# Optimization experiments

Measured on AMD Instinct MI355X. Metric: run time of the kernel, lower is better.

Reference implementation:

```python
import jax, jax.numpy as jnp
import numpy as np

ALPHA = 0.2  # LeakyReLU negative slope (init arg alpha)


def setup_inputs() -> dict:
    key = jax.random.key(0)
    k1, k2, k3 = jax.random.split(key, 3)
    B, N, F_in, F_out = 8, 2048, 256, 256
    inp = jax.random.normal(k1, (B, N, F_in), dtype=jnp.float32)
    adj = jnp.ones((B, N, N), dtype=jnp.float32)  # unused by the module's forward
    # xavier_uniform with gain=1.414
    gain = 1.414
    bW = gain * np.sqrt(6.0 / (F_in + F_out))
    W = jax.random.uniform(k2, (F_in, F_out), minval=-bW, maxval=bW, dtype=jnp.float32)
    ba = gain * np.sqrt(6.0 / (2 * F_out + 1))
    a = jax.random.uniform(k3, (2 * F_out, 1), minval=-ba, maxval=ba, dtype=jnp.float32)
    return {"inp": inp, "adj": adj, "W": W, "a": a}


def reference(inp, adj, W, a):
    # inp: [B, N, F_in]; W: [F_in, F_out]; a: [2*F_out, 1]. adj is unused (as in source).
    F_out = W.shape[1]
    h = jnp.matmul(inp, W)  # [B, N, F_out]
    # e[b,i,j] = leakyrelu(a1 . h_i + a2 . h_j)  (equivalent to the repeat+cat+matmul)
    a1 = a[:F_out, 0]
    a2 = a[F_out:, 0]
    s1 = jnp.einsum('bnf,f->bn', h, a1)  # [B, N]
    s2 = jnp.einsum('bnf,f->bn', h, a2)  # [B, N]
    e = jax.nn.leaky_relu(s1[:, :, None] + s2[:, None, :], negative_slope=ALPHA)  # [B, N, N]
    # global per-batch min-max normalization, then affine *30 - 20
    mn = jnp.min(e, axis=(1, 2), keepdims=True)
    mx = jnp.max(e, axis=(1, 2), keepdims=True)
    e = (e - mn) / (mx - mn) * 30.0 - 20.0
    attention = jax.nn.sigmoid(e)  # dropout p=0 / eval: identity
    h_prime = jnp.matmul(attention, h)  # [B, N, F_out]
    h_prime = jax.nn.elu(h_prime)  # concat=True branch
    return h_prime, attention
```

## Files before the change

kernel.cpp:

```cpp
#include <hip/hip_runtime.h>
#include <stdint.h>

#define B_   8
#define N_   2048
#define F_   256
#define BN_  (B_ * N_)
#define ALPHA_ 0.2f

typedef __attribute__((ext_vector_type(8))) short  short8;
typedef __attribute__((ext_vector_type(4))) float  f32x4;

__device__ __forceinline__ unsigned short f2bf(float x) {
  uint32_t u = __float_as_uint(x);
  uint32_t r = (u + 0x7fffu + ((u >> 16) & 1u)) >> 16;
  return (unsigned short)r;
}

__device__ __forceinline__ uint32_t fkey(float f) {
  uint32_t b = __float_as_uint(f);
  return b ^ (uint32_t)(((int32_t)b >> 31) | (int32_t)0x80000000);
}
__device__ __forceinline__ float ikey(uint32_t k) {
  uint32_t b = (k & 0x80000000u) ? (k ^ 0x80000000u) : ~k;
  return __uint_as_float(b);
}

__device__ __forceinline__ void async_load16(const void* g, void* l) {
  __builtin_amdgcn_global_load_lds(
      (const __attribute__((address_space(1))) uint32_t*)g,
      (__attribute__((address_space(3))) uint32_t*)l, 16, 0, 0);
}

__device__ __forceinline__ void nt_store4(float* p, f32x4 v) {
  __builtin_nontemporal_store(v, (f32x4*)p);
}

__global__ void k_cvt_w(const float* __restrict__ W, unsigned short* __restrict__ WT,
                        uint32_t* __restrict__ maxk, uint32_t* __restrict__ mink) {
  int k = blockIdx.x, n = threadIdx.x;
  if (k == 0 && n < 16) { maxk[n] = 0u; mink[n] = 0xFFFFFFFFu; }
  WT[n * F_ + k] = f2bf(W[k * F_ + n]);
}

__launch_bounds__(256, 2)
__global__ void k_gemm1(const float* __restrict__ inp,
                        const unsigned short* __restrict__ WT,
                        const float* __restrict__ avec,
                        unsigned short* __restrict__ hT,
                        float* __restrict__ s1g, float* __restrict__ s2g,
                        uint32_t* __restrict__ maxk, uint32_t* __restrict__ mink) {
  __shared__ __align__(16) char smem[256 * 72 * 2];
  __shared__ float s1_lds[64], s2_lds[64];
  unsigned short* Atile = (unsigned short*)smem;
  unsigned short* Btile = (unsigned short*)(smem + 4096);

  const int tid  = threadIdx.x;
  const int wave = tid >> 6, lane = tid & 63;
  const int n16  = lane & 15, quad = lane >> 4;
  const int i0   = blockIdx.x * 64;
  const int b    = i0 >> 11;

  if (tid < 64) { s1_lds[tid] = 0.0f; s2_lds[tid] = 0.0f; }

  f32x4 acc[4][4];
  #pragma unroll
  for (int mt = 0; mt < 4; ++mt)
    #pragma unroll
    for (int nt = 0; nt < 4; ++nt) acc[mt][nt] = (f32x4){0.f, 0.f, 0.f, 0.f};

  for (int k0 = 0; k0 < F_; k0 += 32) {
    {
      int r = tid >> 2, cp = tid & 3;
      const float* gp = inp + (size_t)(i0 + r) * F_ + k0 + cp * 8;
      float4 va = *(const float4*)gp;
      float4 vb = *(const float4*)(gp + 4);
      short8 sv;
      sv[0] = (short)f2bf(va.x); sv[1] = (short)f2bf(va.y);
      sv[2] = (short)f2bf(va.z); sv[3] = (short)f2bf(va.w);
      sv[4] = (short)f2bf(vb.x); sv[5] = (short)f2bf(vb.y);
      sv[6] = (short)f2bf(vb.z); sv[7] = (short)f2bf(vb.w);
      *(short8*)((char*)Atile + r * 64 + cp * 16) = sv;
    }
    #pragma unroll
    for (int g4 = 0; g4 < 4; ++g4) {
      int f = (wave << 6) + (g4 << 4) + (lane >> 2);
      int p = lane & 3;
      async_load16(WT + (size_t)f * F_ + k0 + p * 8,
                   (char*)Btile + wave * 4096 + g4 * 1024);
    }
    __syncthreads();

    short8 af[4], bf_[4];
    #pragma unroll
    for (int mt = 0; mt < 4; ++mt)
      af[mt] = *(const short8*)((const char*)Atile + ((mt * 16 + n16) * 64 + quad * 16));
    #pragma unroll
    for (int nt = 0; nt < 4; ++nt)
      bf_[nt] = *(const short8*)((const char*)Btile + ((wave * 64 + nt * 16 + n16) * 64 + quad * 16));
    #pragma unroll
    for (int mt = 0; mt < 4; ++mt)
      #pragma unroll
      for (int nt = 0; nt < 4; ++nt)
        acc[mt][nt] = __builtin_amdgcn_mfma_f32_16x16x32_bf16(af[mt], bf_[nt], acc[mt][nt], 0, 0, 0);
    __syncthreads();
  }

  unsigned short* Trans = (unsigned short*)smem;

  #pragma unroll
  for (int mt = 0; mt < 4; ++mt)
    #pragma unroll
    for (int nt = 0; nt < 4; ++nt) {
      int f = (wave << 6) + (nt << 4) + n16;
      int i = (mt << 4) + (quad << 2);
      ushort4 pk;
      pk.x = f2bf(acc[mt][nt][0]); pk.y = f2bf(acc[mt][nt][1]);
      pk.z = f2bf(acc[mt][nt][2]); pk.w = f2bf(acc[mt][nt][3]);
      *(ushort4*)(Trans + f * 72 + i) = pk;
    }

  float a1v[4], a2v[4];
  #pragma unroll
  for (int nt = 0; nt < 4; ++nt) {
    int f = (wave << 6) + (nt << 4) + n16;
    a1v[nt] = avec[f];
    a2v[nt] = avec[F_ + f];
  }
  #pragma unroll
  for (int mt = 0; mt < 4; ++mt) {
    float s1p[4] = {0, 0, 0, 0}, s2p[4] = {0, 0, 0, 0};
    #pragma unroll
    for (int nt = 0; nt < 4; ++nt)
      #pragma unroll
      for (int rg = 0; rg < 4; ++rg) {
        s1p[rg] = fmaf(acc[mt][nt][rg], a1v[nt], s1p[rg]);
        s2p[rg] = fmaf(acc[mt][nt][rg], a2v[nt], s2p[rg]);
      }
    #pragma unroll
    for (int rg = 0; rg < 4; ++rg) {
      float v1 = s1p[rg], v2 = s2p[rg];
      #pragma unroll
      for (int off = 1; off < 16; off <<= 1) {
        v1 += __shfl_xor(v1, off);
        v2 += __shfl_xor(v2, off);
      }
      if (n16 == 0) {
        atomicAdd(&s1_lds[(mt << 4) + (quad << 2) + rg], v1);
        atomicAdd(&s2_lds[(mt << 4) + (quad << 2) + rg], v2);
      }
    }
  }
  __syncthreads();

  #pragma unroll
  for (int it = 0; it < 8; ++it) {
    int f = it * 32 + wave * 8 + (lane >> 3);
    int i = (lane & 7) * 8;
    short8 v = *(const short8*)(Trans + f * 72 + i);
    *(short8*)(hT + (size_t)f * BN_ + i0 + i) = v;
  }

  if (tid < 64) {
    float v1 = s1_lds[tid], v2 = s2_lds[tid];
    s1g[i0 + tid] = v1;
    s2g[i0 + tid] = v2;
    float mn1 = v1, mx1 = v1, mn2 = v2, mx2 = v2;
    #pragma unroll
    for (int off = 1; off < 64; off <<= 1) {
      mn1 = fminf(mn1, __shfl_xor(mn1, off));
      mx1 = fmaxf(mx1, __shfl_xor(mx1, off));
      mn2 = fminf(mn2, __shfl_xor(mn2, off));
      mx2 = fmaxf(mx2, __shfl_xor(mx2, off));
    }
    if (tid == 0) {
      atomicMax(&maxk[b * 2 + 0], fkey(mx1));
      atomicMax(&maxk[b * 2 + 1], fkey(mx2));
      atomicMin(&mink[b * 2 + 0], fkey(mn1));
      atomicMin(&mink[b * 2 + 1], fkey(mn2));
    }
  }
}

__launch_bounds__(256, 2)
__global__ void k_gemm2(const unsigned short* __restrict__ hT,
                        const float* __restrict__ s1, const float* __restrict__ s2,
                        const uint32_t* __restrict__ maxk, const uint32_t* __restrict__ mink,
                        float* __restrict__ hprime,
                        float* __restrict__ att) {
  __shared__ __align__(16) unsigned short Btile[3][256 * 32];
  __shared__ __align__(16) unsigned short Atile[2][1024];
  __shared__ __align__(16) float s2_lds[N_];

  const int tid  = threadIdx.x;
  const int wave = tid >> 6, lane = tid & 63;
  const int n16  = lane & 15, quad = lane >> 4;
  const int blk  = blockIdx.x;
  const int b    = blk & 7;
  const int i0   = (blk >> 3) * 32;

  float mx1 = ikey(maxk[b * 2 + 0]), mx2 = ikey(maxk[b * 2 + 1]);
  float mn1 = ikey(mink[b * 2 + 0]), mn2 = ikey(mink[b * 2 + 1]);
  float smn = mn1 + mn2, smx = mx1 + mx2;
  float emn = fmaxf(smn, ALPHA_ * smn);
  float emx = fmaxf(smx, ALPHA_ * smx);
  float scale  = 30.0f / (emx - emn);
  const float uscale = -scale;
  const float ubias  = emn * scale + 20.0f;

  const int r_att = tid >> 3;
  const int c_att = tid & 7;
  const float s1v = s1[b * N_ + i0 + r_att];
  const float* s2b = s2 + b * N_;
  float* attrow = att + ((size_t)(b * N_ + i0 + r_att)) * N_;

  auto stage_b = [&](int slot, int k0_) {
    #pragma unroll
    for (int g4 = 0; g4 < 4; ++g4) {
      int f = (wave << 6) + (g4 << 4) + (lane >> 2);
      int p = lane & 3;
      async_load16(hT + (size_t)f * BN_ + b * N_ + k0_ + p * 8,
                   (char*)Btile + slot * 16384 + wave * 4096 + g4 * 1024);
    }
  };

  #pragma unroll
  for (int it = 0; it < 2; ++it)
    async_load16(s2b + wave * 512 + it * 256 + lane * 4,
                 (char*)s2_lds + wave * 2048 + it * 1024);
  stage_b(0, 0);
  stage_b(1, 32);
  asm volatile("s_waitcnt vmcnt(8)" ::: "memory");
  __builtin_amdgcn_s_barrier();
  asm volatile("" ::: "memory");

  f32x4 acc[2][4];
  #pragma unroll
  for (int mt = 0; mt < 2; ++mt)
    #pragma unroll
    for (int nt = 0; nt < 4; ++nt) acc[mt][nt] = (f32x4){0.f, 0.f, 0.f, 0.f};

  int sl_r = 0, sl_n = 2;
  for (int t = 0; t < 64; ++t) {
    const int abuf = (t & 1) * 2048;
    const int k0   = t << 5;

    float4 va = *(const float4*)((const char*)s2_lds + k0 * 4 + c_att * 16);
    float v[4] = {va.x, va.y, va.z, va.w};
    #pragma unroll
    for (int jj = 0; jj < 4; ++jj) {
      float s = s1v + v[jj];
      float l = fmaxf(s, ALPHA_ * s);
      float u = fmaf(l, uscale, ubias);
      float p_ = __builtin_amdgcn_rcpf(1.0f + __expf(u));
      v[jj] = p_;
    }
    nt_store4(attrow + k0 + c_att * 4, (f32x4){v[0], v[1], v[2], v[3]});
    ushort4 spk;
    spk.x = f2bf(v[0]); spk.y = f2bf(v[1]); spk.z = f2bf(v[2]); spk.w = f2bf(v[3]);
    *(ushort4*)((char*)Atile + abuf + tid * 8) = spk;

    asm volatile("s_waitcnt vmcnt(5) lgkmcnt(0)" ::: "memory");
    __builtin_amdgcn_s_barrier();
    asm volatile("" ::: "memory");

    stage_b(sl_n, k0 + 64);

    short8 af0 = *(const short8*)((const char*)Atile + abuf + n16 * 64 + quad * 16);
    short8 af1 = *(const short8*)((const char*)Atile + abuf + (16 + n16) * 64 + quad * 16);
    short8 bf_[4];
    #pragma unroll
    for (int nt = 0; nt < 4; ++nt)
      bf_[nt] = *(const short8*)((const char*)Btile + sl_r * 16384 +
                                 (wave * 64 + nt * 16 + n16) * 64 + quad * 16);

    #pragma unroll
    for (int nt = 0; nt < 4; ++nt) {
      acc[0][nt] = __builtin_amdgcn_mfma_f32_16x16x32_bf16(af0, bf_[nt], acc[0][nt], 0, 0, 0);
      acc[1][nt] = __builtin_amdgcn_mfma_f32_16x16x32_bf16(af1, bf_[nt], acc[1][nt], 0, 0, 0);
    }

    sl_r = (sl_r == 2) ? 0 : sl_r + 1;
    sl_n = (sl_n == 2) ? 0 : sl_n + 1;
  }

  asm volatile("s_waitcnt vmcnt(0)" ::: "memory");

  float* hp = hprime + ((size_t)(b * N_ + i0)) * F_;
  #pragma unroll
  for (int mt = 0; mt < 2; ++mt)
    #pragma unroll
    for (int nt = 0; nt < 4; ++nt) {
      int fcol = (wave << 6) + (nt << 4) + n16;
      int irow = (mt << 4) + (quad << 2);
      #pragma unroll
      for (int rg = 0; rg < 4; ++rg) {
        float x = acc[mt][nt][rg];
        float y = x > 0.0f ? x : (__expf(x) - 1.0f);
        __builtin_nontemporal_store(y, hp + (size_t)(irow + rg) * F_ + fcol);
      }
    }
}

extern "C" void kernel_launch(void* const* d_in, const int* in_sizes, int n_in,
                              void* d_out, int out_size, void* d_ws, size_t ws_size,
                              hipStream_t stream) {
  const float* inp  = (const float*)d_in[0];
  const float* W    = (const float*)d_in[2];
  const float* avec = (const float*)d_in[3];

  float* hprime = (float*)d_out;
  float* att    = (float*)d_out + (size_t)B_ * N_ * F_;

  char* ws = (char*)d_ws;
  unsigned short* WT = (unsigned short*)ws;
  unsigned short* hT = (unsigned short*)(ws + 131072);
  float* s1          = (float*)(ws + 131072 + 8388608);
  float* s2          = s1 + BN_;
  uint32_t* maxk     = (uint32_t*)(s2 + BN_);
  uint32_t* mink     = maxk + 16;

  k_cvt_w<<<F_, F_, 0, stream>>>(W, WT, maxk, mink);
  k_gemm1<<<BN_ / 64, 256, 0, stream>>>(inp, WT, avec, hT, s1, s2, maxk, mink);
  k_gemm2<<<512, 256, 0, stream>>>(hT, s1, s2, maxk, mink, hprime, att);
}
```

Measured before the change: 272.7 us.

## Compute attention fragments in registers per wave, drop block barriers in gemm2 loop

Reworks the attention-times-h GEMM so each wave builds its own MFMA A-operand directly in registers from s1/s2, instead of writing bf16 attention to shared memory and synchronising the block every k-step. Each wave now owns a 16x128 output tile and stages its own private double-buffered slice of hT, which removes the per-iteration block barrier. The cost is redundant sigmoid computation, since two waves share each row and each computes the full A fragment. The sequence also becomes more serial: the next tile is loaded while only a single buffer is in flight, and waits on vmcnt(1) may expose load latency.

```diff
diff --git a/kernel.cpp b/kernel.cpp
--- a/kernel.cpp
+++ b/kernel.cpp
@@ -187,13 +187,13 @@
                         const uint32_t* __restrict__ maxk, const uint32_t* __restrict__ mink,
                         float* __restrict__ hprime,
                         float* __restrict__ att) {
-  __shared__ __align__(16) unsigned short Btile[3][256 * 32];
-  __shared__ __align__(16) unsigned short Atile[2][1024];
+  __shared__ __align__(16) char Btile[4 * 2 * 8192];
   __shared__ __align__(16) float s2_lds[N_];
 
   const int tid  = threadIdx.x;
   const int wave = tid >> 6, lane = tid & 63;
   const int n16  = lane & 15, quad = lane >> 4;
+  const int wm   = wave >> 1, wn = wave & 1;
   const int blk  = blockIdx.x;
   const int b    = blk & 7;
   const int i0   = (blk >> 3) * 32;
@@ -207,19 +207,20 @@
   const float uscale = -scale;
   const float ubias  = emn * scale + 20.0f;
 
-  const int r_att = tid >> 3;
-  const int c_att = tid & 7;
-  const float s1v = s1[b * N_ + i0 + r_att];
-  const float* s2b = s2 + b * N_;
-  float* attrow = att + ((size_t)(b * N_ + i0 + r_att)) * N_;
-
-  auto stage_b = [&](int slot, int k0_) {
-    #pragma unroll
-    for (int g4 = 0; g4 < 4; ++g4) {
-      int f = (wave << 6) + (g4 << 4) + (lane >> 2);
+  const int   myrow = 16 * wm + n16;
+  const float s1v   = s1[b * N_ + i0 + myrow];
+  const float* s2b  = s2 + b * N_;
+  float* attrow = att + ((size_t)(b * N_ + i0 + myrow)) * N_;
+
+  char* wseg = Btile + wave * 16384;
+
+  auto stage_b = [&](int buf_, int k0_) {
+    #pragma unroll
+    for (int g = 0; g < 8; ++g) {
+      int f = 128 * wn + g * 16 + (lane >> 2);
       int p = lane & 3;
       async_load16(hT + (size_t)f * BN_ + b * N_ + k0_ + p * 8,
-                   (char*)Btile + slot * 16384 + wave * 4096 + g4 * 1024);
+                   wseg + buf_ * 8192 + g * 1024);
     }
   };
 
@@ -228,77 +229,63 @@
     async_load16(s2b + wave * 512 + it * 256 + lane * 4,
                  (char*)s2_lds + wave * 2048 + it * 1024);
   stage_b(0, 0);
-  stage_b(1, 32);
   asm volatile("s_waitcnt vmcnt(8)" ::: "memory");
   __builtin_amdgcn_s_barrier();
-  asm volatile("" ::: "memory");
-
-  f32x4 acc[2][4];
-  #pragma unroll
-  for (int mt = 0; mt < 2; ++mt)
-    #pragma unroll
-    for (int nt = 0; nt < 4; ++nt) acc[mt][nt] = (f32x4){0.f, 0.f, 0.f, 0.f};
-
-  int sl_r = 0, sl_n = 2;
+  asm volatile("s_waitcnt vmcnt(0)" ::: "memory");
+
+  f32x4 acc[8];
+  #pragma unroll
+  for (int nt = 0; nt < 8; ++nt) acc[nt] = (f32x4){0.f, 0.f, 0.f, 0.f};
+
   for (int t = 0; t < 64; ++t) {
-    const int abuf = (t & 1) * 2048;
-    const int k0   = t << 5;
-
-    float4 va = *(const float4*)((const char*)s2_lds + k0 * 4 + c_att * 16);
-    float v[4] = {va.x, va.y, va.z, va.w};
-    #pragma unroll
-    for (int jj = 0; jj < 4; ++jj) {
+    const int cur = t & 1;
+    const int k0  = t << 5;
+
+    asm volatile("s_waitcnt vmcnt(1)" ::: "memory");
+
+    short8 bf_[8];
+    #pragma unroll
+    for (int nt = 0; nt < 8; ++nt)
+      bf_[nt] = *(const short8*)(wseg + cur * 8192 + (nt * 16 + n16) * 64 + quad * 16);
+
+    if (t < 63) stage_b(cur ^ 1, k0 + 32);
+
+    float4 va = *(const float4*)((const char*)s2_lds + (k0 + quad * 8) * 4);
+    float4 vb = *(const float4*)((const char*)s2_lds + (k0 + quad * 8) * 4 + 16);
+    float v[8] = {va.x, va.y, va.z, va.w, vb.x, vb.y, vb.z, vb.w};
+    #pragma unroll
+    for (int jj = 0; jj < 8; ++jj) {
       float s = s1v + v[jj];
       float l = fmaxf(s, ALPHA_ * s);
       float u = fmaf(l, uscale, ubias);
-      float p_ = __builtin_amdgcn_rcpf(1.0f + __expf(u));
-      v[jj] = p_;
-    }
-    nt_store4(attrow + k0 + c_att * 4, (f32x4){v[0], v[1], v[2], v[3]});
-    ushort4 spk;
-    spk.x = f2bf(v[0]); spk.y = f2bf(v[1]); spk.z = f2bf(v[2]); spk.w = f2bf(v[3]);
-    *(ushort4*)((char*)Atile + abuf + tid * 8) = spk;
-
-    asm volatile("s_waitcnt vmcnt(5) lgkmcnt(0)" ::: "memory");
-    __builtin_amdgcn_s_barrier();
-    asm volatile("" ::: "memory");
-
-    stage_b(sl_n, k0 + 64);
-
-    short8 af0 = *(const short8*)((const char*)Atile + abuf + n16 * 64 + quad * 16);
-    short8 af1 = *(const short8*)((const char*)Atile + abuf + (16 + n16) * 64 + quad * 16);
-    short8 bf_[4];
-    #pragma unroll
-    for (int nt = 0; nt < 4; ++nt)
-      bf_[nt] = *(const short8*)((const char*)Btile + sl_r * 16384 +
-                                 (wave * 64 + nt * 16 + n16) * 64 + quad * 16);
-
-    #pragma unroll
-    for (int nt = 0; nt < 4; ++nt) {
-      acc[0][nt] = __builtin_amdgcn_mfma_f32_16x16x32_bf16(af0, bf_[nt], acc[0][nt], 0, 0, 0);
-      acc[1][nt] = __builtin_amdgcn_mfma_f32_16x16x32_bf16(af1, bf_[nt], acc[1][nt], 0, 0, 0);
-    }
-
-    sl_r = (sl_r == 2) ? 0 : sl_r + 1;
-    sl_n = (sl_n == 2) ? 0 : sl_n + 1;
-  }
-
-  asm volatile("s_waitcnt vmcnt(0)" ::: "memory");
+      v[jj] = __builtin_amdgcn_rcpf(1.0f + __expf(u));
+    }
+    if (wn == 0) nt_store4(attrow + k0 + quad * 8,     (f32x4){v[0], v[1], v[2], v[3]});
+    else         nt_store4(attrow + k0 + quad * 8 + 4, (f32x4){v[4], v[5], v[6], v[7]});
+
+    short8 af;
+    af[0] = (short)f2bf(v[0]); af[1] = (short)f2bf(v[1]);
+    af[2] = (short)f2bf(v[2]); af[3] = (short)f2bf(v[3]);
+    af[4] = (short)f2bf(v[4]); af[5] = (short)f2bf(v[5]);
+    af[6] = (short)f2bf(v[6]); af[7] = (short)f2bf(v[7]);
+
+    #pragma unroll
+    for (int nt = 0; nt < 8; ++nt)
+      acc[nt] = __builtin_amdgcn_mfma_f32_16x16x32_bf16(af, bf_[nt], acc[nt], 0, 0, 0);
+  }
 
   float* hp = hprime + ((size_t)(b * N_ + i0)) * F_;
   #pragma unroll
-  for (int mt = 0; mt < 2; ++mt)
-    #pragma unroll
-    for (int nt = 0; nt < 4; ++nt) {
-      int fcol = (wave << 6) + (nt << 4) + n16;
-      int irow = (mt << 4) + (quad << 2);
-      #pragma unroll
-      for (int rg = 0; rg < 4; ++rg) {
-        float x = acc[mt][nt][rg];
-        float y = x > 0.0f ? x : (__expf(x) - 1.0f);
-        __builtin_nontemporal_store(y, hp + (size_t)(irow + rg) * F_ + fcol);
-      }
-    }
+  for (int nt = 0; nt < 8; ++nt) {
+    int fcol = 128 * wn + nt * 16 + n16;
+    int irow = 16 * wm + quad * 4;
+    #pragma unroll
+    for (int rg = 0; rg < 4; ++rg) {
+      float x = acc[nt][rg];
+      float y = x > 0.0f ? x : (__expf(x) - 1.0f);
+      __builtin_nontemporal_store(y, hp + (size_t)(irow + rg) * F_ + fcol);
+    }
+  }
 }
 
 extern "C" void kernel_launch(void* const* d_in, const int* in_sizes, int n_in,
```

Measured after the change: 344.4 us. 26.3% more time.
